# Optimization experiments

Hardware: AMD Instinct MI355X
Metric: run time of the kernel (lower is better)

Reference implementation:

```python
import jax, jax.numpy as jnp
import numpy as np

BN_EPS = 1e-5

def conv1x1(x, w, b):
    # x: [B,C,H,W], w: [O,C], b: [O]
    return jnp.einsum('bchw,oc->bohw', x, w) + b[None, :, None, None]

def bn_inf(x, gamma, beta, mean, var):
    inv = gamma / jnp.sqrt(var + BN_EPS)
    return (x - mean[None, :, None, None]) * inv[None, :, None, None] + beta[None, :, None, None]

def setup_inputs() -> dict:
    key = jax.random.key(0)
    ks = jax.random.split(key, 24)
    B, Fg, Fl, Fi = 8, 256, 256, 64
    H = W = 64
    c8 = Fi // 8
    d = {}
    d['g'] = jax.random.normal(ks[0], (B, Fg, H, W), jnp.float32)
    d['x'] = jax.random.normal(ks[1], (B, Fl, H, W), jnp.float32)
    # W_g: conv1x1 + BN
    d['Wg_w'] = jax.random.normal(ks[2], (Fi, Fg), jnp.float32) * (1.0 / np.sqrt(Fg))
    d['Wg_b'] = jax.random.normal(ks[3], (Fi,), jnp.float32) * 0.02
    d['bng_gamma'] = jax.random.uniform(ks[4], (Fi,), jnp.float32, 0.5, 1.5)
    d['bng_beta'] = jax.random.normal(ks[5], (Fi,), jnp.float32) * 0.1
    d['bng_mean'] = jax.random.normal(ks[6], (Fi,), jnp.float32) * 0.1
    d['bng_var'] = jax.random.uniform(ks[7], (Fi,), jnp.float32, 0.5, 1.5)
    # W_x: conv1x1 + BN
    d['Wx_w'] = jax.random.normal(ks[8], (Fi, Fl), jnp.float32) * (1.0 / np.sqrt(Fl))
    d['Wx_b'] = jax.random.normal(ks[9], (Fi,), jnp.float32) * 0.02
    d['bnx_gamma'] = jax.random.uniform(ks[10], (Fi,), jnp.float32, 0.5, 1.5)
    d['bnx_beta'] = jax.random.normal(ks[11], (Fi,), jnp.float32) * 0.1
    d['bnx_mean'] = jax.random.normal(ks[12], (Fi,), jnp.float32) * 0.1
    d['bnx_var'] = jax.random.uniform(ks[13], (Fi,), jnp.float32, 0.5, 1.5)
    # psi: conv1x1 (Fi->1) + BN(1) + sigmoid
    d['psi_w'] = jax.random.normal(ks[14], (1, Fi), jnp.float32) * (1.0 / np.sqrt(Fi))
    d['psi_b'] = jax.random.normal(ks[15], (1,), jnp.float32) * 0.02
    d['bnp_gamma'] = jax.random.uniform(ks[16], (1,), jnp.float32, 0.5, 1.5)
    d['bnp_beta'] = jax.random.normal(ks[17], (1,), jnp.float32) * 0.1
    d['bnp_mean'] = jax.random.normal(ks[18], (1,), jnp.float32) * 0.1
    d['bnp_var'] = jax.random.uniform(ks[19], (1,), jnp.float32, 0.5, 1.5)
    # PAM convs
    d['pb_w'] = jax.random.normal(ks[20], (c8, Fi), jnp.float32) * (1.0 / np.sqrt(Fi))
    d['pb_b'] = jnp.zeros((c8,), jnp.float32)
    d['pc_w'] = jax.random.normal(ks[21], (c8, Fi), jnp.float32) * (1.0 / np.sqrt(Fi))
    d['pc_b'] = jnp.zeros((c8,), jnp.float32)
    d['pd_w'] = jax.random.normal(ks[22], (Fi, Fi), jnp.float32) * (1.0 / np.sqrt(Fi))
    d['pd_b'] = jnp.zeros((Fi,), jnp.float32)
    # scalar gates (torch inits to 0; use small nonzero to exercise the path)
    d['alpha'] = jax.random.normal(ks[23], (1,), jnp.float32) * 0.05
    d['cam_beta'] = jax.random.normal(jax.random.fold_in(key, 99), (1,), jnp.float32) * 0.05
    return d

def _cam(psi, cam_beta):
    B, C, H, W = psi.shape
    feat = psi.reshape(B, C, H * W)                       # [B,C,HW]
    att = jnp.einsum('bcn,bdn->bcd', feat, feat)          # [B,C,C]
    att_new = jnp.max(att, axis=-1, keepdims=True) - att  # max-subtract trick
    att = jax.nn.softmax(att_new, axis=-1)
    out = jnp.einsum('bcd,bdn->bcn', att, feat).reshape(B, C, H, W)
    return cam_beta[0] * out + psi

def _pam(psi, pb_w, pb_b, pc_w, pc_b, pd_w, pd_b, alpha):
    B, C, H, W = psi.shape
    HW = H * W
    fb = conv1x1(psi, pb_w, pb_b).reshape(B, -1, HW)      # [B,C/8,HW]
    fc = conv1x1(psi, pc_w, pc_b).reshape(B, -1, HW)      # [B,C/8,HW]
    energy = jnp.einsum('bki,bkj->bij', fb, fc)           # [B,HW,HW]
    att = jax.nn.softmax(energy, axis=-1)
    fd = conv1x1(psi, pd_w, pd_b).reshape(B, C, HW)       # [B,C,HW]
    out = jnp.einsum('bcj,bij->bci', fd, att).reshape(B, C, H, W)
    return alpha[0] * out + psi

def reference(g, x, Wg_w, Wg_b, bng_gamma, bng_beta, bng_mean, bng_var,
              Wx_w, Wx_b, bnx_gamma, bnx_beta, bnx_mean, bnx_var,
              psi_w, psi_b, bnp_gamma, bnp_beta, bnp_mean, bnp_var,
              pb_w, pb_b, pc_w, pc_b, pd_w, pd_b, alpha, cam_beta):
    g1 = bn_inf(conv1x1(g, Wg_w, Wg_b), bng_gamma, bng_beta, bng_mean, bng_var)
    x1 = bn_inf(conv1x1(x, Wx_w, Wx_b), bnx_gamma, bnx_beta, bnx_mean, bnx_var)
    psi = jax.nn.relu(g1 + x1)                            # [B,F_int,H,W]
    cam = _cam(psi, cam_beta)
    pam = _pam(psi, pb_w, pb_b, pc_w, pc_b, pd_w, pd_b, alpha)
    gate = bn_inf(conv1x1(cam * pam, psi_w, psi_b), bnp_gamma, bnp_beta, bnp_mean, bnp_var)
    da = jax.nn.sigmoid(gate)                             # [B,1,H,W]
    return x * da
```

## Files before the change

### kernel.cpp

```cpp
#include <hip/hip_runtime.h>
#include <hip/hip_bf16.h>
#include <math.h>

#define BB 8
#define CIN 256
#define FI 64
#define HW 4096
#define C8 8
#define EPS 1e-5f
#define LOG2E 1.4426950408889634f

typedef __attribute__((ext_vector_type(8))) short bf16x8;
typedef __attribute__((ext_vector_type(4))) float f32x4;
typedef unsigned short u16;

static __device__ __forceinline__ u16 f2b(float x) {
    unsigned u = __builtin_bit_cast(unsigned, x);
    return (u16)((u + 0x8000u) >> 16);
}
static __device__ __forceinline__ unsigned pk2(float a, float b) {
    unsigned ua = __builtin_bit_cast(unsigned, a);
    unsigned ub = __builtin_bit_cast(unsigned, b);
    return ((ua + 0x8000u) >> 16) | ((ub + 0x8000u) & 0xffff0000u);
}
static __device__ __forceinline__ unsigned cvtpk(float a, float b) {
    unsigned r;
    asm("v_cvt_pk_bf16_f32 %0, %1, %2" : "=v"(r) : "v"(a), "v"(b));
    return r;
}
static __device__ __forceinline__ float b2f(u16 v) {
    return __builtin_bit_cast(float, ((unsigned)v) << 16);
}

__global__ __launch_bounds__(256) void k_prep(
    const float* __restrict__ Wg, const float* __restrict__ Wgb,
    const float* __restrict__ gg, const float* __restrict__ gbeta,
    const float* __restrict__ gm, const float* __restrict__ gv,
    const float* __restrict__ Wx, const float* __restrict__ Wxb,
    const float* __restrict__ xg, const float* __restrict__ xbeta,
    const float* __restrict__ xm, const float* __restrict__ xv,
    const float* __restrict__ pbw, const float* __restrict__ pbb,
    const float* __restrict__ pcw, const float* __restrict__ pcb,
    const float* __restrict__ pdw, const float* __restrict__ pdb,
    u16* __restrict__ Wp, float* __restrict__ Cp,
    u16* __restrict__ Wcat, float* __restrict__ bcat)
{
    const int gid = blockIdx.x * 256 + threadIdx.x;
    for (int idx = gid; idx < FI * 512; idx += 4096) {
        int o = idx >> 9, k = idx & 511;
        float s, w;
        if (k < 256) { s = gg[o] * rsqrtf(gv[o] + EPS); w = Wg[o * 256 + k]; }
        else         { s = xg[o] * rsqrtf(xv[o] + EPS); w = Wx[o * 256 + k - 256]; }
        Wp[idx] = f2b(w * s);
    }
    for (int idx = gid; idx < 80 * 64; idx += 4096) {
        int row = idx >> 6, col = idx & 63;
        float w;
        if (row < 8)       w = pbw[row * 64 + col] * LOG2E;
        else if (row < 16) w = pcw[(row - 8) * 64 + col];
        else               w = pdw[(row - 16) * 64 + col];
        Wcat[idx] = f2b(w);
    }
    if (blockIdx.x == 0) {
        int tid = threadIdx.x;
        if (tid < FI) {
            float ig = gg[tid] * rsqrtf(gv[tid] + EPS);
            float ix = xg[tid] * rsqrtf(xv[tid] + EPS);
            Cp[tid] = (Wgb[tid] - gm[tid]) * ig + gbeta[tid]
                    + (Wxb[tid] - xm[tid]) * ix + xbeta[tid];
        }
        if (tid >= 64 && tid < 144) {
            int r = tid - 64;
            float bv = (r < 8) ? pbb[r] * LOG2E : (r < 16 ? pcb[r - 8] : pdb[r - 16]);
            bcat[r] = bv;
        }
    }
}

__global__ __launch_bounds__(256) void k_psi(
    const float* __restrict__ g, const float* __restrict__ x,
    const u16* __restrict__ Wp, const float* __restrict__ Cp,
    const u16* __restrict__ Wcat, const float* __restrict__ bcat,
    u16* __restrict__ psiB, u16* __restrict__ psiLo,
    u16* __restrict__ fbcT, u16* __restrict__ fdB)
{
    const int tid  = threadIdx.x;
    const int lane = tid & 63;
    const int w    = tid >> 6;
    const int n    = lane & 15;
    const int quad = lane >> 4;
    const int b    = blockIdx.y;
    const int p0   = blockIdx.x * 64;

    __shared__ u16 InT[64][72];
    __shared__ u16 Tbc[64][16];

    f32x4 acc[4];
#pragma unroll
    for (int mt = 0; mt < 4; ++mt) acc[mt] = (f32x4){0.f, 0.f, 0.f, 0.f};

    for (int kc = 0; kc < 8; ++kc) {
        const float* src = (kc < 4) ? g : x;
        const int ch0 = (kc & 3) * 64;
        __syncthreads();
#pragma unroll
        for (int r = 0; r < 4; ++r) {
            int ch = (tid >> 4) + r * 16;
            int px = (tid & 15) * 4;
            float4 v = *(const float4*)&src[((size_t)b * CIN + ch0 + ch) * HW + p0 + px];
            InT[px][ch]     = f2b(v.x);
            InT[px + 1][ch] = f2b(v.y);
            InT[px + 2][ch] = f2b(v.z);
            InT[px + 3][ch] = f2b(v.w);
        }
        __syncthreads();
#pragma unroll
        for (int ks = 0; ks < 2; ++ks) {
            const int kglob = kc * 64 + ks * 32;
            bf16x8 bfrag = *(const bf16x8*)&InT[w * 16 + n][ks * 32 + quad * 8];
#pragma unroll
            for (int mt = 0; mt < 4; ++mt) {
                bf16x8 af = *(const bf16x8*)&Wp[(mt * 16 + n) * 512 + kglob + quad * 8];
                acc[mt] = __builtin_amdgcn_mfma_f32_16x16x32_bf16(
                              af, bfrag, acc[mt], 0, 0, 0);
            }
        }
    }

    float pv[4][4];
#pragma unroll
    for (int mt = 0; mt < 4; ++mt)
#pragma unroll
        for (int r = 0; r < 4; ++r) {
            int c = mt * 16 + quad * 4 + r;
            float v = acc[mt][r] + Cp[c];
            v = v > 0.f ? v : 0.f;
            pv[mt][r] = v;
            u16 hb = f2b(v);
            size_t idx = ((size_t)b * FI + c) * HW + p0 + w * 16 + n;
            psiB[idx]  = hb;
            psiLo[idx] = f2b(v - b2f(hb));
        }
    __syncthreads();
#pragma unroll
    for (int mt = 0; mt < 4; ++mt) {
        *(unsigned*)&InT[w * 16 + n][mt * 16 + quad * 4]     = cvtpk(pv[mt][0], pv[mt][1]);
        *(unsigned*)&InT[w * 16 + n][mt * 16 + quad * 4 + 2] = cvtpk(pv[mt][2], pv[mt][3]);
    }
    __syncthreads();

    f32x4 facc[5];
#pragma unroll
    for (int nt = 0; nt < 5; ++nt) facc[nt] = (f32x4){0.f, 0.f, 0.f, 0.f};
#pragma unroll
    for (int ks = 0; ks < 2; ++ks) {
        bf16x8 af = *(const bf16x8*)&InT[w * 16 + n][ks * 32 + quad * 8];
#pragma unroll
        for (int nt = 0; nt < 5; ++nt) {
            bf16x8 bf = *(const bf16x8*)&Wcat[(nt * 16 + n) * FI + ks * 32 + quad * 8];
            facc[nt] = __builtin_amdgcn_mfma_f32_16x16x32_bf16(af, bf, facc[nt], 0, 0, 0);
        }
    }
    __syncthreads();

    {
        float bias = bcat[n];
#pragma unroll
        for (int r = 0; r < 4; ++r)
            Tbc[w * 16 + quad * 4 + r][n] = f2b(facc[0][r] + bias);
    }
#pragma unroll
    for (int nt = 1; nt < 5; ++nt) {
        int ch = (nt - 1) * 16 + n;
        float bias = bcat[nt * 16 + n];
        *(unsigned*)&InT[ch][w * 16 + quad * 4]     = cvtpk(facc[nt][0] + bias, facc[nt][1] + bias);
        *(unsigned*)&InT[ch][w * 16 + quad * 4 + 2] = cvtpk(facc[nt][2] + bias, facc[nt][3] + bias);
    }
    __syncthreads();
    {
        int row = tid >> 2, part = tid & 3;
        uint2 v = *(const uint2*)&Tbc[row][part * 4];
        *(uint2*)&fbcT[((size_t)b * HW + p0 + row) * 16 + part * 4] = v;
    }
#pragma unroll
    for (int rep = 0; rep < 2; ++rep) {
        int t = rep * 256 + tid;
        int ch = t >> 3, seg = t & 7;
        bf16x8 v = *(const bf16x8*)&InT[ch][seg * 8];
        *(bf16x8*)&fdB[((size_t)b * FI + ch) * HW + p0 + seg * 8] = v;
    }
}

__global__ __launch_bounds__(256) void k_gram(
    const u16* __restrict__ psiB, const u16* __restrict__ psiLo,
    float* __restrict__ Gp)
{
    const int tid  = threadIdx.x;
    const int lane = tid & 63;
    const int w    = tid >> 6;
    const int n    = lane & 15;
    const int quad = lane >> 4;
    const int s    = blockIdx.x;
    const int b    = blockIdx.y;

    f32x4 acc[4];
#pragma unroll
    for (int nt = 0; nt < 4; ++nt) acc[nt] = (f32x4){0.f, 0.f, 0.f, 0.f};

    for (int ks = 0; ks < 4; ++ks) {
        const int k0 = s * 128 + ks * 32;
        const size_t ra = ((size_t)b * FI + w * 16 + n) * HW + k0 + quad * 8;
        bf16x8 ah = *(const bf16x8*)&psiB[ra];
        bf16x8 al = *(const bf16x8*)&psiLo[ra];
#pragma unroll
        for (int nt = 0; nt < 4; ++nt) {
            const size_t rb = ((size_t)b * FI + nt * 16 + n) * HW + k0 + quad * 8;
            bf16x8 bh = *(const bf16x8*)&psiB[rb];
            bf16x8 bl = *(const bf16x8*)&psiLo[rb];
            acc[nt] = __builtin_amdgcn_mfma_f32_16x16x32_bf16(ah, bh, acc[nt], 0, 0, 0);
            acc[nt] = __builtin_amdgcn_mfma_f32_16x16x32_bf16(ah, bl, acc[nt], 0, 0, 0);
            acc[nt] = __builtin_amdgcn_mfma_f32_16x16x32_bf16(al, bh, acc[nt], 0, 0, 0);
        }
    }
#pragma unroll
    for (int nt = 0; nt < 4; ++nt)
#pragma unroll
        for (int r = 0; r < 4; ++r) {
            int i = w * 16 + quad * 4 + r;
            Gp[(((size_t)s * 8 + b) * 64 + i) * 64 + nt * 16 + n] = acc[nt][r];
        }
}

__global__ __launch_bounds__(256) void k_camsm(
    const float* __restrict__ Gp, float* __restrict__ att)
{
    const int tid = threadIdx.x, d = tid & 63, ty = tid >> 6;
    const int b = blockIdx.x, grp = blockIdx.y;
#pragma unroll 1
    for (int rr = 0; rr < 4; ++rr) {
        int i = grp * 16 + ty * 4 + rr;
        float gsum = 0.f;
#pragma unroll 1
        for (int s = 0; s < 32; ++s) gsum += Gp[(((size_t)s * 8 + b) * 64 + i) * 64 + d];
        float M = gsum;
#pragma unroll
        for (int msk = 1; msk < 64; msk <<= 1) M = fmaxf(M, __shfl_xor(M, msk));
        float a = M - gsum;
        float m2 = a;
#pragma unroll
        for (int msk = 1; msk < 64; msk <<= 1) m2 = fmaxf(m2, __shfl_xor(m2, msk));
        float p = __expf(a - m2);
        float ssum = p;
#pragma unroll
        for (int msk = 1; msk < 64; msk <<= 1) ssum += __shfl_xor(ssum, msk);
        att[((size_t)b * 64 + i) * 64 + d] = p / ssum;
    }
}

__global__ __launch_bounds__(256) void k_pam(
    const u16* __restrict__ fbcT, const u16* __restrict__ fdB,
    u16* __restrict__ Opart, float* __restrict__ ml)
{
    const int tid  = threadIdx.x;
    const int lane = tid & 63;
    const int w    = tid >> 6;
    const int n    = lane & 15;
    const int quad = lane >> 4;
    const int b    = blockIdx.x;
    const int i0   = blockIdx.y * 64;
    const int p    = blockIdx.z;
    const int jstart = p * 32, jend = jstart + 32;

    __shared__ u16 Ks[68][8];
    __shared__ u16 Qs[64][32];
    __shared__ u16 Vs[64][72];
    __shared__ u16 Ps[4][16][72];

    for (int t = tid; t < 64 * 16; t += 256) ((unsigned*)Qs)[t] = 0u;
    if (tid < 16) ((unsigned*)&Ks[64][0])[tid] = 0u;
    __syncthreads();
    if (tid < 64)
        *(bf16x8*)&Qs[tid][0] = *(const bf16x8*)&fbcT[((size_t)b * HW + i0 + tid) * 16];
    __syncthreads();
    const bf16x8 qfrag = *(const bf16x8*)&Qs[w * 16 + n][quad * 8];

    const int kkey = tid >> 1, khalf = tid & 1;
    const int vch  = tid >> 3, vseg  = tid & 7;

    const u16* kp  = fbcT + ((size_t)b * HW + jstart * 64) * 16;
    const u16* vp  = fdB + (size_t)b * FI * HW + jstart * 64;

    uint2 kreg = make_uint2(0u, 0u);
    bf16x8 vreg0, vreg1;
    {
        if (tid < 128)
            kreg = *(const uint2*)(kp + (size_t)kkey * 16 + 8 + khalf * 4);
        vreg0 = *(const bf16x8*)(vp + (size_t)vch * HW + vseg * 8);
        vreg1 = *(const bf16x8*)(vp + (size_t)(32 + vch) * HW + vseg * 8);
    }

    f32x4 oacc[4];
#pragma unroll
    for (int mt = 0; mt < 4; ++mt) oacc[mt] = (f32x4){0.f, 0.f, 0.f, 0.f};
    float m = -1e30f, l = 0.f;

    for (int jc = jstart; jc < jend; ++jc) {
        __syncthreads();
        if (tid < 128) *(uint2*)&Ks[kkey][khalf * 4] = kreg;
        *(bf16x8*)&Vs[vch][vseg * 8]      = vreg0;
        *(bf16x8*)&Vs[32 + vch][vseg * 8] = vreg1;
        if (jc + 1 < jend) {
            kp += 64 * 16;
            vp += 64;
            if (tid < 128)
                kreg = *(const uint2*)(kp + (size_t)kkey * 16 + 8 + khalf * 4);
            vreg0 = *(const bf16x8*)(vp + (size_t)vch * HW + vseg * 8);
            vreg1 = *(const bf16x8*)(vp + (size_t)(32 + vch) * HW + vseg * 8);
        }
        __syncthreads();

        f32x4 s[4];
#pragma unroll
        for (int mt = 0; mt < 4; ++mt) {
            bf16x8 af = *(const bf16x8*)&Ks[mt * 16 + n + quad][0];
            s[mt] = __builtin_amdgcn_mfma_f32_16x16x32_bf16(
                        af, qfrag, (f32x4){0.f, 0.f, 0.f, 0.f}, 0, 0, 0);
        }

        float cmax = -1e30f;
#pragma unroll
        for (int mt = 0; mt < 4; ++mt)
            cmax = fmaxf(cmax, fmaxf(fmaxf(s[mt][0], s[mt][1]),
                                     fmaxf(s[mt][2], s[mt][3])));
        cmax = fmaxf(cmax, __shfl_xor(cmax, 16));
        cmax = fmaxf(cmax, __shfl_xor(cmax, 32));

        if (__any(cmax > m + 8.f)) {
            float mnew  = fmaxf(m, cmax);
            float scale = __builtin_amdgcn_exp2f(m - mnew);
            l *= scale;
#pragma unroll
            for (int mt = 0; mt < 4; ++mt) {
                oacc[mt][0] *= scale; oacc[mt][1] *= scale;
                oacc[mt][2] *= scale; oacc[mt][3] *= scale;
            }
            m = mnew;
        }

        float psum = 0.f;
        unsigned pw[4][2];
#pragma unroll
        for (int mt = 0; mt < 4; ++mt) {
            float e0 = __builtin_amdgcn_exp2f(s[mt][0] - m);
            float e1 = __builtin_amdgcn_exp2f(s[mt][1] - m);
            float e2 = __builtin_amdgcn_exp2f(s[mt][2] - m);
            float e3 = __builtin_amdgcn_exp2f(s[mt][3] - m);
            psum += (e0 + e1) + (e2 + e3);
            pw[mt][0] = cvtpk(e0, e1);
            pw[mt][1] = cvtpk(e2, e3);
        }
        l += psum;

#pragma unroll
        for (int mt = 0; mt < 4; ++mt)
            *(uint2*)&Ps[w][n][mt * 16 + quad * 4] = make_uint2(pw[mt][0], pw[mt][1]);
        asm volatile("s_waitcnt lgkmcnt(0)" ::: "memory");

#pragma unroll
        for (int k0 = 0; k0 < 2; ++k0) {
            bf16x8 pf = *(const bf16x8*)&Ps[w][n][k0 * 32 + quad * 8];
#pragma unroll
            for (int mt = 0; mt < 4; ++mt) {
                bf16x8 vf = *(const bf16x8*)&Vs[mt * 16 + n][k0 * 32 + quad * 8];
                oacc[mt] = __builtin_amdgcn_mfma_f32_16x16x32_bf16(
                               vf, pf, oacc[mt], 0, 0, 0);
            }
        }
    }

    l += __shfl_xor(l, 16);
    l += __shfl_xor(l, 32);
    const float rl = 1.f / l;
#pragma unroll
    for (int mt = 0; mt < 4; ++mt)
#pragma unroll
        for (int r = 0; r < 4; ++r) {
            int c = mt * 16 + quad * 4 + r;
            Opart[(((size_t)p * 8 + b) * FI + c) * HW + i0 + w * 16 + n] =
                f2b(oacc[mt][r] * rl);
        }
    if (quad == 0)
        ((float2*)ml)[((size_t)p * 8 + b) * HW + i0 + w * 16 + n] = make_float2(m, l);
}

__global__ __launch_bounds__(256) void k_final(
    const u16* __restrict__ psiB, const u16* __restrict__ psiLo,
    const float* __restrict__ att,
    const u16* __restrict__ Opart, const float* __restrict__ ml,
    const float* __restrict__ x,
    const float* __restrict__ psiw, const float* __restrict__ psib,
    const float* __restrict__ pg, const float* __restrict__ pbeta,
    const float* __restrict__ pm, const float* __restrict__ pv,
    const float* __restrict__ alpha, const float* __restrict__ camb,
    float* __restrict__ out)
{
    const int tid = threadIdx.x, tx = tid & 63, ty = tid >> 6;
    const int b = blockIdx.y, p0 = blockIdx.x * 64;
    __shared__ float tp[64][65];
    __shared__ float A[64][64];
    __shared__ float Zp[4][64];

#pragma unroll
    for (int r = 0; r < 16; ++r) {
        int c = ty * 16 + r;
        size_t idx = ((size_t)b * FI + c) * HW + p0 + tx;
        tp[c][tx] = b2f(psiB[idx]) + b2f(psiLo[idx]);
        A[c][tx]  = att[((size_t)b * 64 + c) * 64 + tx];
    }
    __syncthreads();

    float2 ml0 = ((const float2*)ml)[((size_t)0 * 8 + b) * HW + p0 + tx];
    float2 ml1 = ((const float2*)ml)[((size_t)1 * 8 + b) * HW + p0 + tx];
    float M  = fmaxf(ml0.x, ml1.x);
    float w0 = ml0.y * __builtin_amdgcn_exp2f(ml0.x - M);
    float w1 = ml1.y * __builtin_amdgcn_exp2f(ml1.x - M);
    float winv = 1.f / (w0 + w1);
    w0 *= winv; w1 *= winv;

    const float al = alpha[0], cb = camb[0];
    const int c0 = __builtin_amdgcn_readfirstlane(ty * 16);
    float acc[16];
#pragma unroll
    for (int i = 0; i < 16; ++i) acc[i] = 0.f;
#pragma unroll 16
    for (int d = 0; d < 64; ++d) {
        float v = tp[d][tx];
#pragma unroll
        for (int i = 0; i < 16; ++i) acc[i] += A[c0 + i][d] * v;
    }
    float z = 0.f;
#pragma unroll
    for (int i = 0; i < 16; ++i) {
        int c = c0 + i;
        float ps  = tp[c][tx];
        float cam = cb * acc[i] + ps;
        float oa = w0 * b2f(Opart[(((size_t)0 * 8 + b) * FI + c) * HW + p0 + tx])
                 + w1 * b2f(Opart[(((size_t)1 * 8 + b) * FI + c) * HW + p0 + tx]);
        float pam = al * oa + ps;
        z += psiw[c] * (cam * pam);
    }
    Zp[ty][tx] = z;
    __syncthreads();
    float zt = Zp[0][tx] + Zp[1][tx] + Zp[2][tx] + Zp[3][tx] + psib[0];
    float inv = pg[0] * rsqrtf(pv[0] + EPS);
    float gate = (zt - pm[0]) * inv + pbeta[0];
    float da = 1.f / (1.f + __expf(-gate));

#pragma unroll 8
    for (int r = 0; r < 64; ++r) {
        int cl = ty + 4 * r;
        size_t idx = ((size_t)b * CIN + cl) * HW + p0 + tx;
        out[idx] = x[idx] * da;
    }
}

extern "C" void kernel_launch(void* const* d_in, const int* in_sizes, int n_in,
                              void* d_out, int out_size, void* d_ws, size_t ws_size,
                              hipStream_t stream)
{
    const float* g     = (const float*)d_in[0];
    const float* x     = (const float*)d_in[1];
    const float* Wg_w  = (const float*)d_in[2];
    const float* Wg_b  = (const float*)d_in[3];
    const float* bng_g = (const float*)d_in[4];
    const float* bng_b = (const float*)d_in[5];
    const float* bng_m = (const float*)d_in[6];
    const float* bng_v = (const float*)d_in[7];
    const float* Wx_w  = (const float*)d_in[8];
    const float* Wx_b  = (const float*)d_in[9];
    const float* bnx_g = (const float*)d_in[10];
    const float* bnx_b = (const float*)d_in[11];
    const float* bnx_m = (const float*)d_in[12];
    const float* bnx_v = (const float*)d_in[13];
    const float* psi_w = (const float*)d_in[14];
    const float* psi_b = (const float*)d_in[15];
    const float* bnp_g = (const float*)d_in[16];
    const float* bnp_b = (const float*)d_in[17];
    const float* bnp_m = (const float*)d_in[18];
    const float* bnp_v = (const float*)d_in[19];
    const float* pb_w  = (const float*)d_in[20];
    const float* pb_b  = (const float*)d_in[21];
    const float* pc_w  = (const float*)d_in[22];
    const float* pc_b  = (const float*)d_in[23];
    const float* pd_w  = (const float*)d_in[24];
    const float* pd_b  = (const float*)d_in[25];
    const float* alpha = (const float*)d_in[26];
    const float* camb  = (const float*)d_in[27];
    float* out = (float*)d_out;

    float* ws   = (float*)d_ws;
    u16*  psiB  = (u16*)(ws);
    u16*  psiLo = (u16*)(ws + 1048576);
    u16*  fbcT  = (u16*)(ws + 2097152);
    u16*  fdB   = (u16*)(ws + 2359296);
    float* att  = ws + 3407872;
    u16*  Wp    = (u16*)(ws + 3440640);
    float* Cp   = ws + 3457024;
    u16*  Wcat  = (u16*)(ws + 3457088);
    float* bcat = ws + 3459648;
    float* mlws = ws + 3459744;
    float* Gp   = ws + 3590816;
    u16*  Opart = (u16*)(ws + 3590816);

    k_prep<<<dim3(16), 256, 0, stream>>>(Wg_w, Wg_b, bng_g, bng_b, bng_m, bng_v,
                                         Wx_w, Wx_b, bnx_g, bnx_b, bnx_m, bnx_v,
                                         pb_w, pb_b, pc_w, pc_b, pd_w, pd_b,
                                         Wp, Cp, Wcat, bcat);
    k_psi<<<dim3(64, 8), 256, 0, stream>>>(g, x, Wp, Cp, Wcat, bcat,
                                           psiB, psiLo, fbcT, fdB);
    k_gram<<<dim3(32, 8), 256, 0, stream>>>(psiB, psiLo, Gp);
    k_camsm<<<dim3(8, 4), 256, 0, stream>>>(Gp, att);
    k_pam<<<dim3(8, 64, 2), 256, 0, stream>>>(fbcT, fdB, Opart, mlws);
    k_final<<<dim3(64, 8), 256, 0, stream>>>(psiB, psiLo, att, Opart, mlws, x,
                                             psi_w, psi_b, bnp_g, bnp_b, bnp_m, bnp_v,
                                             alpha, camb, out);
}
```

Measured before the change: 292.4 us.

## Load PAM K/V fragments directly from global into registers, dropping LDS staging

The PAM flash-attention loop now skips staging K and V tiles through shared memory. Each wave loads its MFMA operand fragments for K and V straight from global memory into registers, double-buffers the K fragments, and unrolls the loop by two with setprio around the MFMA groups. This removes both block-wide barriers and the LDS store/load round trip per key tile. The cost is that all four waves fetch the same K/V data independently, so global/L2 traffic is higher and loads are less coalesced, and register pressure rises.

```diff
diff --git a/kernel.cpp b/kernel.cpp
--- a/kernel.cpp
+++ b/kernel.cpp
@@ -271,112 +271,110 @@
     const int p    = blockIdx.z;
     const int jstart = p * 32, jend = jstart + 32;
 
-    __shared__ u16 Ks[68][8];
-    __shared__ u16 Qs[64][32];
-    __shared__ u16 Vs[64][72];
     __shared__ u16 Ps[4][16][72];
 
-    for (int t = tid; t < 64 * 16; t += 256) ((unsigned*)Qs)[t] = 0u;
-    if (tid < 16) ((unsigned*)&Ks[64][0])[tid] = 0u;
-    __syncthreads();
-    if (tid < 64)
-        *(bf16x8*)&Qs[tid][0] = *(const bf16x8*)&fbcT[((size_t)b * HW + i0 + tid) * 16];
-    __syncthreads();
-    const bf16x8 qfrag = *(const bf16x8*)&Qs[w * 16 + n][quad * 8];
-
-    const int kkey = tid >> 1, khalf = tid & 1;
-    const int vch  = tid >> 3, vseg  = tid & 7;
-
-    const u16* kp  = fbcT + ((size_t)b * HW + jstart * 64) * 16;
-    const u16* vp  = fdB + (size_t)b * FI * HW + jstart * 64;
-
-    uint2 kreg = make_uint2(0u, 0u);
-    bf16x8 vreg0, vreg1;
-    {
-        if (tid < 128)
-            kreg = *(const uint2*)(kp + (size_t)kkey * 16 + 8 + khalf * 4);
-        vreg0 = *(const bf16x8*)(vp + (size_t)vch * HW + vseg * 8);
-        vreg1 = *(const bf16x8*)(vp + (size_t)(32 + vch) * HW + vseg * 8);
-    }
+    bf16x8 qfrag = {};
+    if (quad == 0)
+        qfrag = *(const bf16x8*)&fbcT[((size_t)b * HW + i0 + w * 16 + n) * 16];
+
+    const u16* kbase = fbcT + (size_t)b * HW * 16 + 8;
+    const u16* vbase = fdB + ((size_t)b * FI + n) * HW + quad * 8;
 
     f32x4 oacc[4];
 #pragma unroll
     for (int mt = 0; mt < 4; ++mt) oacc[mt] = (f32x4){0.f, 0.f, 0.f, 0.f};
     float m = -1e30f, l = 0.f;
 
-    for (int jc = jstart; jc < jend; ++jc) {
-        __syncthreads();
-        if (tid < 128) *(uint2*)&Ks[kkey][khalf * 4] = kreg;
-        *(bf16x8*)&Vs[vch][vseg * 8]      = vreg0;
-        *(bf16x8*)&Vs[32 + vch][vseg * 8] = vreg1;
-        if (jc + 1 < jend) {
-            kp += 64 * 16;
-            vp += 64;
-            if (tid < 128)
-                kreg = *(const uint2*)(kp + (size_t)kkey * 16 + 8 + khalf * 4);
-            vreg0 = *(const bf16x8*)(vp + (size_t)vch * HW + vseg * 8);
-            vreg1 = *(const bf16x8*)(vp + (size_t)(32 + vch) * HW + vseg * 8);
-        }
-        __syncthreads();
-
-        f32x4 s[4];
-#pragma unroll
-        for (int mt = 0; mt < 4; ++mt) {
-            bf16x8 af = *(const bf16x8*)&Ks[mt * 16 + n + quad][0];
-            s[mt] = __builtin_amdgcn_mfma_f32_16x16x32_bf16(
-                        af, qfrag, (f32x4){0.f, 0.f, 0.f, 0.f}, 0, 0, 0);
-        }
-
-        float cmax = -1e30f;
-#pragma unroll
-        for (int mt = 0; mt < 4; ++mt)
-            cmax = fmaxf(cmax, fmaxf(fmaxf(s[mt][0], s[mt][1]),
-                                     fmaxf(s[mt][2], s[mt][3])));
-        cmax = fmaxf(cmax, __shfl_xor(cmax, 16));
-        cmax = fmaxf(cmax, __shfl_xor(cmax, 32));
-
-        if (__any(cmax > m + 8.f)) {
-            float mnew  = fmaxf(m, cmax);
-            float scale = __builtin_amdgcn_exp2f(m - mnew);
-            l *= scale;
-#pragma unroll
-            for (int mt = 0; mt < 4; ++mt) {
-                oacc[mt][0] *= scale; oacc[mt][1] *= scale;
-                oacc[mt][2] *= scale; oacc[mt][3] *= scale;
-            }
-            m = mnew;
-        }
-
-        float psum = 0.f;
-        unsigned pw[4][2];
-#pragma unroll
-        for (int mt = 0; mt < 4; ++mt) {
-            float e0 = __builtin_amdgcn_exp2f(s[mt][0] - m);
-            float e1 = __builtin_amdgcn_exp2f(s[mt][1] - m);
-            float e2 = __builtin_amdgcn_exp2f(s[mt][2] - m);
-            float e3 = __builtin_amdgcn_exp2f(s[mt][3] - m);
-            psum += (e0 + e1) + (e2 + e3);
-            pw[mt][0] = cvtpk(e0, e1);
-            pw[mt][1] = cvtpk(e2, e3);
-        }
-        l += psum;
-
-#pragma unroll
-        for (int mt = 0; mt < 4; ++mt)
-            *(uint2*)&Ps[w][n][mt * 16 + quad * 4] = make_uint2(pw[mt][0], pw[mt][1]);
-        asm volatile("s_waitcnt lgkmcnt(0)" ::: "memory");
-
-#pragma unroll
-        for (int k0 = 0; k0 < 2; ++k0) {
-            bf16x8 pf = *(const bf16x8*)&Ps[w][n][k0 * 32 + quad * 8];
-#pragma unroll
-            for (int mt = 0; mt < 4; ++mt) {
-                bf16x8 vf = *(const bf16x8*)&Vs[mt * 16 + n][k0 * 32 + quad * 8];
-                oacc[mt] = __builtin_amdgcn_mfma_f32_16x16x32_bf16(
-                               vf, pf, oacc[mt], 0, 0, 0);
-            }
-        }
-    }
+    bf16x8 kc0, kc1, kc2, kc3;
+    {
+        const u16* kp = kbase + (size_t)(jstart * 64 + n) * 16;
+        kc0 = *(const bf16x8*)(kp);
+        kc1 = *(const bf16x8*)(kp + 256);
+        kc2 = *(const bf16x8*)(kp + 512);
+        kc3 = *(const bf16x8*)(kp + 768);
+    }
+    bf16x8 kn0, kn1, kn2, kn3;
+
+#define PAM_BODY(KA0, KA1, KA2, KA3, KB0, KB1, KB2, KB3, JC)                    \
+    {                                                                           \
+        const int j0 = (JC) * 64;                                               \
+                  \
+        bf16x8 vf[8];                                                           \
+        _Pragma("unroll")                                                       \
+        for (int mt = 0; mt < 4; ++mt) {                                        \
+            vf[mt * 2]     = *(const bf16x8*)(vbase + (size_t)mt * (16 * HW) + j0);      \
+            vf[mt * 2 + 1] = *(const bf16x8*)(vbase + (size_t)mt * (16 * HW) + j0 + 32); \
+        }                                                                       \
+                                                                 \
+        f32x4 s[4];                                                             \
+        __builtin_amdgcn_s_setprio(1);                                          \
+        s[0] = __builtin_amdgcn_mfma_f32_16x16x32_bf16(KA0, qfrag, (f32x4){0.f,0.f,0.f,0.f}, 0, 0, 0); \
+        s[1] = __builtin_amdgcn_mfma_f32_16x16x32_bf16(KA1, qfrag, (f32x4){0.f,0.f,0.f,0.f}, 0, 0, 0); \
+        s[2] = __builtin_amdgcn_mfma_f32_16x16x32_bf16(KA2, qfrag, (f32x4){0.f,0.f,0.f,0.f}, 0, 0, 0); \
+        s[3] = __builtin_amdgcn_mfma_f32_16x16x32_bf16(KA3, qfrag, (f32x4){0.f,0.f,0.f,0.f}, 0, 0, 0); \
+        __builtin_amdgcn_s_setprio(0);                                          \
+                        \
+        if ((JC) + 1 < jend) {                                                  \
+            const u16* kp = kbase + (size_t)(((JC) + 1) * 64 + n) * 16;         \
+            KB0 = *(const bf16x8*)(kp);                                         \
+            KB1 = *(const bf16x8*)(kp + 256);                                   \
+            KB2 = *(const bf16x8*)(kp + 512);                                   \
+            KB3 = *(const bf16x8*)(kp + 768);                                   \
+        }                                                                       \
+        float cmax = -1e30f;                                                    \
+        _Pragma("unroll")                                                       \
+        for (int mt = 0; mt < 4; ++mt)                                          \
+            cmax = fmaxf(cmax, fmaxf(fmaxf(s[mt][0], s[mt][1]),                 \
+                                     fmaxf(s[mt][2], s[mt][3])));               \
+        cmax = fmaxf(cmax, __shfl_xor(cmax, 16));                               \
+        cmax = fmaxf(cmax, __shfl_xor(cmax, 32));                               \
+        if (__any(cmax > m + 8.f)) {                                            \
+            float mnew  = fmaxf(m, cmax);                                       \
+            float scale = __builtin_amdgcn_exp2f(m - mnew);                     \
+            l *= scale;                                                         \
+            _Pragma("unroll")                                                   \
+            for (int mt = 0; mt < 4; ++mt) {                                    \
+                oacc[mt][0] *= scale; oacc[mt][1] *= scale;                     \
+                oacc[mt][2] *= scale; oacc[mt][3] *= scale;                     \
+            }                                                                   \
+            m = mnew;                                                           \
+        }                                                                       \
+        float psum = 0.f;                                                       \
+        unsigned pw[4][2];                                                      \
+        _Pragma("unroll")                                                       \
+        for (int mt = 0; mt < 4; ++mt) {                                        \
+            float e0 = __builtin_amdgcn_exp2f(s[mt][0] - m);                    \
+            float e1 = __builtin_amdgcn_exp2f(s[mt][1] - m);                    \
+            float e2 = __builtin_amdgcn_exp2f(s[mt][2] - m);                    \
+            float e3 = __builtin_amdgcn_exp2f(s[mt][3] - m);                    \
+            psum += (e0 + e1) + (e2 + e3);                                      \
+            pw[mt][0] = cvtpk(e0, e1);                                          \
+            pw[mt][1] = cvtpk(e2, e3);                                          \
+        }                                                                       \
+        l += psum;                                                              \
+        _Pragma("unroll")                                                       \
+        for (int mt = 0; mt < 4; ++mt)                                          \
+            *(uint2*)&Ps[w][n][mt * 16 + quad * 4] = make_uint2(pw[mt][0], pw[mt][1]); \
+        asm volatile("s_waitcnt lgkmcnt(0)" ::: "memory");                      \
+        __builtin_amdgcn_sched_barrier(0);                                      \
+        __builtin_amdgcn_s_setprio(1);                                          \
+        _Pragma("unroll")                                                       \
+        for (int k0 = 0; k0 < 2; ++k0) {                                        \
+            bf16x8 pf = *(const bf16x8*)&Ps[w][n][k0 * 32 + quad * 8];          \
+            _Pragma("unroll")                                                   \
+            for (int mt = 0; mt < 4; ++mt) {                                    \
+                oacc[mt] = __builtin_amdgcn_mfma_f32_16x16x32_bf16(             \
+                               vf[mt * 2 + k0], pf, oacc[mt], 0, 0, 0);         \
+            }                                                                   \
+        }                                                                       \
+        __builtin_amdgcn_s_setprio(0);                                          \
+    }
+
+    for (int jc = jstart; jc < jend; jc += 2) {
+        PAM_BODY(kc0, kc1, kc2, kc3, kn0, kn1, kn2, kn3, jc)
+        PAM_BODY(kn0, kn1, kn2, kn3, kc0, kc1, kc2, kc3, jc + 1)
+    }
+#undef PAM_BODY
 
     l += __shfl_xor(l, 16);
     l += __shfl_xor(l, 32);
```

New measurement: 365.6 us. 25.1% more time.

## Double-buffer K/V tiles in PAM kernel with XOR-swizzled LDS and priority hints

Applied to the files above, without the earlier changes.

The PAM attention kernel now double-buffers its K and V shared-memory tiles, so each iteration needs only one barrier instead of two. The V and P tiles move from padded rows to XOR-swizzled 64-wide rows to avoid LDS bank conflicts without padding. The Q fragment is loaded straight from global memory into registers, with zero-fill for the upper quads, instead of being staged through shared memory. s_setprio hints and a sched_barrier wrap the MFMA phases, and the price is extra LDS for the second buffers.

```diff
diff --git a/kernel.cpp b/kernel.cpp
--- a/kernel.cpp
+++ b/kernel.cpp
@@ -17,11 +17,6 @@
 static __device__ __forceinline__ u16 f2b(float x) {
     unsigned u = __builtin_bit_cast(unsigned, x);
     return (u16)((u + 0x8000u) >> 16);
-}
-static __device__ __forceinline__ unsigned pk2(float a, float b) {
-    unsigned ua = __builtin_bit_cast(unsigned, a);
-    unsigned ub = __builtin_bit_cast(unsigned, b);
-    return ((ua + 0x8000u) >> 16) | ((ub + 0x8000u) & 0xffff0000u);
 }
 static __device__ __forceinline__ unsigned cvtpk(float a, float b) {
     unsigned r;
@@ -271,61 +266,61 @@
     const int p    = blockIdx.z;
     const int jstart = p * 32, jend = jstart + 32;
 
-    __shared__ u16 Ks[68][8];
-    __shared__ u16 Qs[64][32];
-    __shared__ u16 Vs[64][72];
-    __shared__ u16 Ps[4][16][72];
-
-    for (int t = tid; t < 64 * 16; t += 256) ((unsigned*)Qs)[t] = 0u;
-    if (tid < 16) ((unsigned*)&Ks[64][0])[tid] = 0u;
-    __syncthreads();
-    if (tid < 64)
-        *(bf16x8*)&Qs[tid][0] = *(const bf16x8*)&fbcT[((size_t)b * HW + i0 + tid) * 16];
-    __syncthreads();
-    const bf16x8 qfrag = *(const bf16x8*)&Qs[w * 16 + n][quad * 8];
+    __shared__ u16 Ks[2][68][8];
+    __shared__ u16 Vs[2][64][64];
+    __shared__ u16 Ps[4][16][64];
+
+    if (tid < 16) {
+        ((unsigned*)&Ks[0][64][0])[tid] = 0u;
+        ((unsigned*)&Ks[1][64][0])[tid] = 0u;
+    }
+
+    bf16x8 qfrag = {};
+    if (quad == 0)
+        qfrag = *(const bf16x8*)&fbcT[((size_t)b * HW + i0 + w * 16 + n) * 16];
 
     const int kkey = tid >> 1, khalf = tid & 1;
     const int vch  = tid >> 3, vseg  = tid & 7;
-
-    const u16* kp  = fbcT + ((size_t)b * HW + jstart * 64) * 16;
-    const u16* vp  = fdB + (size_t)b * FI * HW + jstart * 64;
+    const int vslot = (vseg ^ (vch & 7)) << 3;
+    const int pswz  = n & 7;
+
+    const u16* kp = fbcT + ((size_t)b * HW + jstart * 64) * 16 + 8;
+    const u16* vp = fdB + (size_t)b * FI * HW + jstart * 64;
 
     uint2 kreg = make_uint2(0u, 0u);
     bf16x8 vreg0, vreg1;
-    {
-        if (tid < 128)
-            kreg = *(const uint2*)(kp + (size_t)kkey * 16 + 8 + khalf * 4);
-        vreg0 = *(const bf16x8*)(vp + (size_t)vch * HW + vseg * 8);
-        vreg1 = *(const bf16x8*)(vp + (size_t)(32 + vch) * HW + vseg * 8);
-    }
+    if (tid < 128) kreg = *(const uint2*)(kp + (size_t)kkey * 16 + khalf * 4);
+    vreg0 = *(const bf16x8*)(vp + (size_t)vch * HW + vseg * 8);
+    vreg1 = *(const bf16x8*)(vp + (size_t)(32 + vch) * HW + vseg * 8);
 
     f32x4 oacc[4];
 #pragma unroll
     for (int mt = 0; mt < 4; ++mt) oacc[mt] = (f32x4){0.f, 0.f, 0.f, 0.f};
     float m = -1e30f, l = 0.f;
 
+    int cur = 0;
     for (int jc = jstart; jc < jend; ++jc) {
-        __syncthreads();
-        if (tid < 128) *(uint2*)&Ks[kkey][khalf * 4] = kreg;
-        *(bf16x8*)&Vs[vch][vseg * 8]      = vreg0;
-        *(bf16x8*)&Vs[32 + vch][vseg * 8] = vreg1;
+        if (tid < 128) *(uint2*)&Ks[cur][kkey][khalf * 4] = kreg;
+        *(bf16x8*)&Vs[cur][vch][vslot]      = vreg0;
+        *(bf16x8*)&Vs[cur][32 + vch][vslot] = vreg1;
         if (jc + 1 < jend) {
             kp += 64 * 16;
             vp += 64;
-            if (tid < 128)
-                kreg = *(const uint2*)(kp + (size_t)kkey * 16 + 8 + khalf * 4);
+            if (tid < 128) kreg = *(const uint2*)(kp + (size_t)kkey * 16 + khalf * 4);
             vreg0 = *(const bf16x8*)(vp + (size_t)vch * HW + vseg * 8);
             vreg1 = *(const bf16x8*)(vp + (size_t)(32 + vch) * HW + vseg * 8);
         }
         __syncthreads();
 
         f32x4 s[4];
+        __builtin_amdgcn_s_setprio(1);
 #pragma unroll
         for (int mt = 0; mt < 4; ++mt) {
-            bf16x8 af = *(const bf16x8*)&Ks[mt * 16 + n + quad][0];
+            bf16x8 af = *(const bf16x8*)&Ks[cur][mt * 16 + n + quad][0];
             s[mt] = __builtin_amdgcn_mfma_f32_16x16x32_bf16(
                         af, qfrag, (f32x4){0.f, 0.f, 0.f, 0.f}, 0, 0, 0);
         }
+        __builtin_amdgcn_s_setprio(0);
 
         float cmax = -1e30f;
 #pragma unroll
@@ -362,20 +357,27 @@
         l += psum;
 
 #pragma unroll
-        for (int mt = 0; mt < 4; ++mt)
-            *(uint2*)&Ps[w][n][mt * 16 + quad * 4] = make_uint2(pw[mt][0], pw[mt][1]);
+        for (int mt = 0; mt < 4; ++mt) {
+            int so = (((mt * 2 + (quad >> 1)) ^ pswz) << 3) + ((quad & 1) << 2);
+            *(uint2*)&Ps[w][n][so] = make_uint2(pw[mt][0], pw[mt][1]);
+        }
         asm volatile("s_waitcnt lgkmcnt(0)" ::: "memory");
-
+        __builtin_amdgcn_sched_barrier(0);
+
+        __builtin_amdgcn_s_setprio(1);
 #pragma unroll
         for (int k0 = 0; k0 < 2; ++k0) {
-            bf16x8 pf = *(const bf16x8*)&Ps[w][n][k0 * 32 + quad * 8];
+            bf16x8 pf = *(const bf16x8*)&Ps[w][n][((k0 * 4 + quad) ^ pswz) << 3];
 #pragma unroll
             for (int mt = 0; mt < 4; ++mt) {
-                bf16x8 vf = *(const bf16x8*)&Vs[mt * 16 + n][k0 * 32 + quad * 8];
+                bf16x8 vf = *(const bf16x8*)
+                    &Vs[cur][mt * 16 + n][((k0 * 4 + quad) ^ pswz) << 3];
                 oacc[mt] = __builtin_amdgcn_mfma_f32_16x16x32_bf16(
                                vf, pf, oacc[mt], 0, 0, 0);
             }
         }
+        __builtin_amdgcn_s_setprio(0);
+        cur ^= 1;
     }
 
     l += __shfl_xor(l, 16);
```

New measurement: 290.2 us. About the same (-0.7%).
